# Kernel optimization log

Measured on AMD Instinct MI355X. Metric: run time of the kernel, lower is better.

## Reference

```python
import jax, jax.numpy as jnp
import numpy as np

B = 8192      # batch (num nodes)
D = 256       # embedding dim
K = 8         # positives per node -> nnz = B*K
EPS = 1e-8


def setup_inputs() -> dict:
    key = jax.random.key(0)
    k_emb, k_val = jax.random.split(key)
    embeddings = jax.random.normal(k_emb, (B, D), dtype=jnp.float32)
    # structured sparse positive mask: node i is positive with (i+1..i+K) mod B
    # -> unique pairs, row-major sorted (coalesced), no self loops
    rows = jnp.repeat(jnp.arange(B, dtype=jnp.int64), K)           # [B*K]
    offs = jnp.tile(jnp.arange(1, K + 1, dtype=jnp.int64), B)      # [B*K]
    cols = (rows + offs) % B
    pos_vals = jax.random.uniform(k_val, (B * K,), dtype=jnp.float32)
    temperature = jnp.float32(0.5)  # learnable scalar nn.Parameter
    return {
        "embeddings": embeddings,
        "pos_vals": pos_vals,
        "temperature": temperature,
        "pos_row": rows,
        "pos_col": cols,
    }


def reference(embeddings, pos_vals, temperature, pos_row, pos_col):
    n = embeddings.shape[0]
    # F.normalize(p=2, dim=1) with eps=1e-12
    norm = jnp.linalg.norm(embeddings, axis=1, keepdims=True)
    z = embeddings / jnp.maximum(norm, 1e-12)

    temp = jax.nn.softplus(temperature)
    sim = jnp.matmul(z, z.T) / temp                                 # [B,B]
    sim = sim - jax.lax.stop_gradient(jnp.max(sim, axis=1, keepdims=True))

    pos_dense = jnp.zeros((n, n), dtype=bool).at[pos_row, pos_col].set(True)
    identity = jnp.eye(n, dtype=bool)
    neg_mask = (~pos_dense) & (~identity)

    # pos weights: 'inverse_sim' -> 1 - values, min-max normalized
    pos_w = 1.0 - pos_vals
    pos_w = (pos_w - jnp.min(pos_w)) / (jnp.max(pos_w) - jnp.min(pos_w) + EPS)

    # neg weights: 'inverse_sim' -> min-max over negative sims, +1; weight_mat=1 elsewhere
    neg_min = jnp.min(jnp.where(neg_mask, sim, jnp.inf))
    neg_max = jnp.max(jnp.where(neg_mask, sim, -jnp.inf))
    neg_w = (sim - neg_min) / (neg_max - neg_min + EPS) + 1.0
    log_weight = jnp.where(neg_mask, jnp.log(neg_w), 0.0)

    log_probs = sim - jax.nn.logsumexp(sim + log_weight, axis=1, keepdims=True)

    pos_log = log_probs[pos_row, pos_col]   # same ordering as torch boolean index (coalesced mask)
    loss = -jnp.mean(pos_log * pos_w)
    return loss
```

## Files before the change

kernel.cpp:

```cpp
#include <hip/hip_runtime.h>

#define NB 8192
#define ND 256
#define NMASK 8191
#define CEPS 1e-8f
#define L2E 1.4426950408889634f
#define LN2 0.6931471805599453f
#define SC1 0x7F7F7F7F

#if __has_builtin(__builtin_amdgcn_exp2f)
#define EXP2(x) __builtin_amdgcn_exp2f(x)
#else
#define EXP2(x) exp2f(x)
#endif

typedef float f32x4 __attribute__((ext_vector_type(4)));
typedef int v8i __attribute__((ext_vector_type(8)));
typedef int v4i __attribute__((ext_vector_type(4)));
union V8 { v8i v; v4i q[2]; };


__global__ void k_norm(const float* __restrict__ emb, const float* __restrict__ temperature,
                       const float* __restrict__ pos_vals, char* __restrict__ zb8,
                       float* __restrict__ bpvmin, float* __restrict__ bpvmax,
                       float* __restrict__ out) {
  const int tid = threadIdx.x, lane = tid & 63, w = tid >> 6;
  const int bid = blockIdx.x;
  if (bid == 0 && tid == 0) out[0] = 0.f;
  float sp = log1pf(expf(temperature[0]));
  float alpha = sqrtf(L2E / sp);
  int row = bid * 4 + w;
  const float4 e = *(const float4*)(emb + row * ND + lane * 4);
  float ss = e.x * e.x + e.y * e.y + e.z * e.z + e.w * e.w;
#pragma unroll
  for (int mk = 1; mk < 64; mk <<= 1) ss += __shfl_xor(ss, mk, 64);
  float rn = alpha / fmaxf(sqrtf(ss), 1e-12f);
  int pk = __builtin_amdgcn_cvt_pk_fp8_f32(e.x * rn, e.y * rn, 0, 0);
  pk = __builtin_amdgcn_cvt_pk_fp8_f32(e.z * rn, e.w * rn, pk, 1);
  *(int*)(zb8 + row * 256 + lane * 4) = pk;
  if (w == 0) {
    float v = (lane < 32) ? pos_vals[bid * 32 + lane] : 0.f;
    float mn = (lane < 32) ? v : INFINITY;
    float mx = (lane < 32) ? v : -INFINITY;
#pragma unroll
    for (int mk = 1; mk < 32; mk <<= 1) {
      mn = fminf(mn, __shfl_xor(mn, mk, 64));
      mx = fmaxf(mx, __shfl_xor(mx, mk, 64));
    }
    if (lane == 0) { bpvmin[bid] = mn; bpvmax[bid] = mx; }
  }
}

__global__ __launch_bounds__(256) void k_gemm(
    const char* __restrict__ zb8, float2* __restrict__ EpR, float2* __restrict__ EpC,
    float* __restrict__ sBand, float* __restrict__ bmin, float* __restrict__ bmax) {
  __shared__ __align__(16) char smem[16384];
  const int tid = threadIdx.x, lane = tid & 63, w = tid >> 6;
  const int l15 = lane & 15, lq = lane >> 4;
  const int bid = blockIdx.x;
  int d, rb;
  if (bid < 2048) { d = bid >> 6; rb = bid & 63; }
  else { d = 32; rb = bid - 2048; }
  const int cb = (rb + d) & 63;
  const int roww = rb * 128 + w * 32;
  const int colbase = cb * 128;

  V8 aF[2][2];
#pragma unroll
  for (int mt = 0; mt < 2; ++mt) {
    const char* ar = zb8 + (roww + mt * 16 + l15) * 256 + lq * 32;
#pragma unroll
    for (int kc = 0; kc < 2; ++kc) {
      aF[mt][kc].q[0] = *(const v4i*)(ar + kc * 128);
      aF[mt][kc].q[1] = *(const v4i*)(ar + kc * 128 + 16);
    }
  }

  float E1r[8], Ear[8];
#pragma unroll
  for (int i = 0; i < 8; ++i) { E1r[i] = 0.f; Ear[i] = 0.f; }
  float2 cA[4][2];
#pragma unroll
  for (int s = 0; s < 4; ++s) { cA[s][0] = make_float2(0.f, 0.f); cA[s][1] = make_float2(0.f, 0.f); }
  float vmn = INFINITY, vmx = -INFINITY;

  const char* gsrc[2];
#pragma unroll
  for (int i = 0; i < 2; ++i) {
    int j = w * 2 + i, T = j >> 1, h = j & 1, nt = T & 1, kc = T >> 1;
    gsrc[i] = zb8 + (colbase + nt * 16 + l15) * 256 + kc * 128 + lq * 32 + h * 16;
  }
#pragma unroll
  for (int i = 0; i < 2; ++i)
    __builtin_amdgcn_global_load_lds(
        (const __attribute__((address_space(1))) void*)(gsrc[i]),
        (__attribute__((address_space(3))) void*)(smem + (w * 2 + i) * 1024), 16, 0, 0);

#pragma unroll
  for (int step = 0; step < 4; ++step) {
    __syncthreads();
    if (step < 3) {
      char* ld = smem + ((step + 1) & 1) * 8192;
#pragma unroll
      for (int i = 0; i < 2; ++i)
        __builtin_amdgcn_global_load_lds(
            (const __attribute__((address_space(1))) void*)(gsrc[i] + (step + 1) * 8192),
            (__attribute__((address_space(3))) void*)(ld + (w * 2 + i) * 1024), 16, 0, 0);
    }
    const char* buf = smem + (step & 1) * 8192;
    f32x4 acc[2][2];
#pragma unroll
    for (int mt = 0; mt < 2; ++mt) {
      acc[mt][0] = (f32x4){0.f, 0.f, 0.f, 0.f};
      acc[mt][1] = (f32x4){0.f, 0.f, 0.f, 0.f};
    }
#pragma unroll
    for (int kc = 0; kc < 2; ++kc) {
      V8 b0, b1;
      b0.q[0] = *(const v4i*)(buf + (kc * 2 + 0) * 2048 + lane * 16);
      b0.q[1] = *(const v4i*)(buf + (kc * 2 + 0) * 2048 + 1024 + lane * 16);
      b1.q[0] = *(const v4i*)(buf + (kc * 2 + 1) * 2048 + lane * 16);
      b1.q[1] = *(const v4i*)(buf + (kc * 2 + 1) * 2048 + 1024 + lane * 16);
#pragma unroll
      for (int mt = 0; mt < 2; ++mt) {
        acc[mt][0] = __builtin_amdgcn_mfma_scale_f32_16x16x128_f8f6f4(
            aF[mt][kc].v, b0.v, acc[mt][0], 0, 0, 0, SC1, 0, SC1);
        acc[mt][1] = __builtin_amdgcn_mfma_scale_f32_16x16x128_f8f6f4(
            aF[mt][kc].v, b1.v, acc[mt][1], 0, 0, 0, SC1, 0, SC1);
      }
    }
    const int offbase = (colbase + step * 32 + l15) - (roww + lq * 4);
    if (d >= 2) {
#pragma unroll
      for (int mt = 0; mt < 2; ++mt)
#pragma unroll
        for (int nt = 0; nt < 2; ++nt)
#pragma unroll
          for (int reg = 0; reg < 4; ++reg) {
            float t = acc[mt][nt][reg];
            float e = EXP2(t);
            E1r[mt * 4 + reg] += e;
            Ear[mt * 4 + reg] = fmaf(e, t, Ear[mt * 4 + reg]);
            cA[step][nt].x += e;
            cA[step][nt].y = fmaf(e, t, cA[step][nt].y);
            vmn = fminf(vmn, t);
            vmx = fmaxf(vmx, t);
          }
    } else if (d == 1) {
#pragma unroll
      for (int mt = 0; mt < 2; ++mt)
#pragma unroll
        for (int nt = 0; nt < 2; ++nt)
#pragma unroll
          for (int reg = 0; reg < 4; ++reg) {
            float t = acc[mt][nt][reg];
            float e = EXP2(t);
            E1r[mt * 4 + reg] += e;
            Ear[mt * 4 + reg] = fmaf(e, t, Ear[mt * 4 + reg]);
            cA[step][nt].x += e;
            cA[step][nt].y = fmaf(e, t, cA[step][nt].y);
            vmn = fminf(vmn, t);
            vmx = fmaxf(vmx, t);
            int off = (offbase + (nt - mt) * 16 - reg) & NMASK;
            if (off <= 8)
              sBand[(roww + mt * 16 + lq * 4 + reg) * 12 + off] = t;
          }
    } else {
#pragma unroll
      for (int mt = 0; mt < 2; ++mt)
#pragma unroll
        for (int nt = 0; nt < 2; ++nt)
#pragma unroll
          for (int reg = 0; reg < 4; ++reg) {
            float t = acc[mt][nt][reg];
            float e = EXP2(t);
            E1r[mt * 4 + reg] += e;
            Ear[mt * 4 + reg] = fmaf(e, t, Ear[mt * 4 + reg]);
            int off = (offbase + (nt - mt) * 16 - reg) & NMASK;
            bool isB = off <= 8;
            vmn = fminf(vmn, isB ? vmn : t);
            vmx = fmaxf(vmx, isB ? vmx : t);
            if (isB)
              sBand[(roww + mt * 16 + lq * 4 + reg) * 12 + off] = t;
          }
    }
  }

#pragma unroll
  for (int mk = 1; mk < 16; mk <<= 1)
#pragma unroll
    for (int i = 0; i < 8; ++i) {
      E1r[i] += __shfl_xor(E1r[i], mk, 64);
      Ear[i] += __shfl_xor(Ear[i], mk, 64);
    }
  if (l15 == 0) {
#pragma unroll
    for (int mt = 0; mt < 2; ++mt)
#pragma unroll
      for (int reg = 0; reg < 4; ++reg) {
        int row = roww + mt * 16 + lq * 4 + reg;
        EpR[d * NB + row] = make_float2(E1r[mt * 4 + reg], Ear[mt * 4 + reg]);
      }
  }
#pragma unroll
  for (int mk = 16; mk < 64; mk <<= 1)
#pragma unroll
    for (int s = 0; s < 4; ++s)
#pragma unroll
      for (int nt = 0; nt < 2; ++nt) {
        cA[s][nt].x += __shfl_xor(cA[s][nt].x, mk, 64);
        cA[s][nt].y += __shfl_xor(cA[s][nt].y, mk, 64);
      }
#pragma unroll
  for (int mk = 1; mk < 64; mk <<= 1) {
    vmn = fminf(vmn, __shfl_xor(vmn, mk, 64));
    vmx = fmaxf(vmx, __shfl_xor(vmx, mk, 64));
  }
  __syncthreads();
  float2* colAcc = (float2*)smem;
  float* redmm = (float*)(smem + 4096);
  if (d != 0 && lq == 0) {
#pragma unroll
    for (int s = 0; s < 4; ++s)
#pragma unroll
      for (int nt = 0; nt < 2; ++nt)
        colAcc[w * 128 + s * 32 + nt * 16 + l15] = cA[s][nt];
  }
  if (lane == 0) { redmm[w] = vmn; redmm[4 + w] = vmx; }
  __syncthreads();
  if (d != 0 && tid < 128) {
    float2 a = colAcc[tid], b = colAcc[128 + tid], c = colAcc[256 + tid], e = colAcc[384 + tid];
    EpC[d * NB + colbase + tid] = make_float2(a.x + b.x + c.x + e.x, a.y + b.y + c.y + e.y);
  }
  if (tid == 0) {
    bmin[bid] = fminf(fminf(redmm[0], redmm[1]), fminf(redmm[2], redmm[3]));
    bmax[bid] = fmaxf(fmaxf(redmm[4], redmm[5]), fmaxf(redmm[6], redmm[7]));
  }
}

__global__ void k_final(const float* __restrict__ pos_vals,
                        const float2* __restrict__ EpR, const float2* __restrict__ EpC,
                        const float* __restrict__ sBand,
                        const float* __restrict__ bmin, const float* __restrict__ bmax,
                        const float* __restrict__ bpvmin, const float* __restrict__ bpvmax,
                        float* __restrict__ out) {
  const int tid = threadIdx.x, lane = tid & 63, w = tid >> 6;
  __shared__ float sv[16];
  __shared__ float coef[4];
  float mn = INFINITY, mx = -INFINITY, pmn = INFINITY, pmx = -INFINITY;
  for (int i = tid; i < 2080; i += 256) { mn = fminf(mn, bmin[i]); mx = fmaxf(mx, bmax[i]); }
  for (int i = tid; i < 2048; i += 256) { pmn = fminf(pmn, bpvmin[i]); pmx = fmaxf(pmx, bpvmax[i]); }
#pragma unroll
  for (int mk = 1; mk < 64; mk <<= 1) {
    mn = fminf(mn, __shfl_xor(mn, mk, 64));
    mx = fmaxf(mx, __shfl_xor(mx, mk, 64));
    pmn = fminf(pmn, __shfl_xor(pmn, mk, 64));
    pmx = fmaxf(pmx, __shfl_xor(pmx, mk, 64));
  }
  if (lane == 0) { sv[w] = mn; sv[4 + w] = mx; sv[8 + w] = pmn; sv[12 + w] = pmx; }
  __syncthreads();
  if (tid == 0) {
    float tmin = fminf(fminf(sv[0], sv[1]), fminf(sv[2], sv[3]));
    float tmax = fmaxf(fmaxf(sv[4], sv[5]), fmaxf(sv[6], sv[7]));
    float pvmin = fminf(fminf(sv[8], sv[9]), fminf(sv[10], sv[11]));
    float pvmax = fmaxf(fmaxf(sv[12], sv[13]), fmaxf(sv[14], sv[15]));
    float At = LN2 / ((tmax - tmin) * LN2 + CEPS);
    coef[0] = At;
    coef[1] = 1.f - At * tmin;
    coef[2] = pvmax;
    coef[3] = 1.f / (pvmax - pvmin + CEPS);
  }
  __syncthreads();
  const float At = coef[0], Bt = coef[1], pvmax = coef[2], pwInv = coef[3];

  int row = blockIdx.x * 256 + tid;
  float e1 = 0.f, ea = 0.f;
#pragma unroll
  for (int dd = 0; dd < 32; ++dd) { float2 p = EpR[dd * NB + row]; e1 += p.x; ea += p.y; }
#pragma unroll
  for (int dd = 1; dd < 32; ++dd) { float2 p = EpC[dd * NB + row]; e1 += p.x; ea += p.y; }
  {
    float2 p = (row < 4096) ? EpR[32 * NB + row] : EpC[32 * NB + row];
    e1 += p.x; ea += p.y;
  }
  float tb[9], Sb = 0.f, Sbt = 0.f;
#pragma unroll
  for (int o = 0; o <= 8; ++o) {
    tb[o] = sBand[row * 12 + o];
    float e = EXP2(tb[o]);
    Sb += e;
    Sbt = fmaf(e, tb[o], Sbt);
  }
  float denom = At * (ea - Sbt) + Bt * (e1 - Sb) + Sb;
  float lse = logf(denom);
  float contrib = 0.f;
#pragma unroll
  for (int k = 0; k < 8; ++k) {
    float v = pos_vals[row * 8 + k];
    contrib += (pvmax - v) * pwInv * (tb[k + 1] * LN2 - lse);
  }
#pragma unroll
  for (int mk = 1; mk < 64; mk <<= 1) contrib += __shfl_xor(contrib, mk, 64);
  __syncthreads();
  if (lane == 0) sv[w] = contrib;
  __syncthreads();
  if (tid == 0)
    atomicAdd(out, -(sv[0] + sv[1] + sv[2] + sv[3]) * (1.0f / 65536.0f));
}

extern "C" void kernel_launch(void* const* d_in, const int* in_sizes, int n_in,
                              void* d_out, int out_size, void* d_ws, size_t ws_size,
                              hipStream_t stream) {
  const float* emb = (const float*)d_in[0];
  const float* pos_vals = (const float*)d_in[1];
  const float* temperature = (const float*)d_in[2];
  float* out = (float*)d_out;

  char* ws = (char*)d_ws;
  size_t off = 0;
  float2* EpR = (float2*)(ws + off); off += (size_t)33 * NB * 8;
  float2* EpC = (float2*)(ws + off); off += (size_t)33 * NB * 8;
  float* sBand = (float*)(ws + off); off += (size_t)NB * 12 * 4;
  float* bmin = (float*)(ws + off); off += 2080 * 4 + 128;
  float* bmax = (float*)(ws + off); off += 2080 * 4 + 128;
  float* bpvmin = (float*)(ws + off); off += 2048 * 4;
  float* bpvmax = (float*)(ws + off); off += 2048 * 4;
  char* zb8 = (char*)(ws + off); off += (size_t)NB * 256;

  k_norm<<<2048, 256, 0, stream>>>(emb, temperature, pos_vals, zb8, bpvmin, bpvmax, out);
  k_gemm<<<2080, 256, 0, stream>>>(zb8, EpR, EpC, sBand, bmin, bmax);
  k_final<<<32, 256, 0, stream>>>(pos_vals, EpR, EpC, sBand, bmin, bmax, bpvmin, bpvmax, out);
}
```

Measured before the change: 103.4 us.

## Load full column tile into LDS upfront, drop double-buffered per-step pipeline

Replaces the double-buffered 4-step LDS pipeline for the B (column) tile with a single bulk load of the whole 128x256 fp8 column tile into 32KB of shared memory, issued before the A fragments are loaded, followed by one barrier. This removes the per-step __syncthreads and interleaved async loads. In exchange LDS use per block doubles, which may reduce occupancy, and compute can no longer overlap with the later loads.

```diff
diff --git a/kernel.cpp b/kernel.cpp
--- a/kernel.cpp
+++ b/kernel.cpp
@@ -54,7 +54,7 @@
 __global__ __launch_bounds__(256) void k_gemm(
     const char* __restrict__ zb8, float2* __restrict__ EpR, float2* __restrict__ EpC,
     float* __restrict__ sBand, float* __restrict__ bmin, float* __restrict__ bmax) {
-  __shared__ __align__(16) char smem[16384];
+  __shared__ __align__(16) char smem[32768];
   const int tid = threadIdx.x, lane = tid & 63, w = tid >> 6;
   const int l15 = lane & 15, lq = lane >> 4;
   const int bid = blockIdx.x;
@@ -65,6 +65,15 @@
   const int roww = rb * 128 + w * 32;
   const int colbase = cb * 128;
 
+#pragma unroll
+  for (int i = 0; i < 8; ++i) {
+    int s = w * 8 + i, T = s >> 1, h = s & 1, ct = T >> 1, kc = T & 1;
+    const char* g = zb8 + (colbase + ct * 16 + l15) * 256 + kc * 128 + lq * 32 + h * 16;
+    __builtin_amdgcn_global_load_lds(
+        (const __attribute__((address_space(1))) void*)(g),
+        (__attribute__((address_space(3))) void*)(smem + s * 1024), 16, 0, 0);
+  }
+
   V8 aF[2][2];
 #pragma unroll
   for (int mt = 0; mt < 2; ++mt) {
@@ -84,30 +93,10 @@
   for (int s = 0; s < 4; ++s) { cA[s][0] = make_float2(0.f, 0.f); cA[s][1] = make_float2(0.f, 0.f); }
   float vmn = INFINITY, vmx = -INFINITY;
 
-  const char* gsrc[2];
-#pragma unroll
-  for (int i = 0; i < 2; ++i) {
-    int j = w * 2 + i, T = j >> 1, h = j & 1, nt = T & 1, kc = T >> 1;
-    gsrc[i] = zb8 + (colbase + nt * 16 + l15) * 256 + kc * 128 + lq * 32 + h * 16;
-  }
-#pragma unroll
-  for (int i = 0; i < 2; ++i)
-    __builtin_amdgcn_global_load_lds(
-        (const __attribute__((address_space(1))) void*)(gsrc[i]),
-        (__attribute__((address_space(3))) void*)(smem + (w * 2 + i) * 1024), 16, 0, 0);
+  __syncthreads();
 
 #pragma unroll
   for (int step = 0; step < 4; ++step) {
-    __syncthreads();
-    if (step < 3) {
-      char* ld = smem + ((step + 1) & 1) * 8192;
-#pragma unroll
-      for (int i = 0; i < 2; ++i)
-        __builtin_amdgcn_global_load_lds(
-            (const __attribute__((address_space(1))) void*)(gsrc[i] + (step + 1) * 8192),
-            (__attribute__((address_space(3))) void*)(ld + (w * 2 + i) * 1024), 16, 0, 0);
-    }
-    const char* buf = smem + (step & 1) * 8192;
     f32x4 acc[2][2];
 #pragma unroll
     for (int mt = 0; mt < 2; ++mt) {
@@ -117,10 +106,12 @@
 #pragma unroll
     for (int kc = 0; kc < 2; ++kc) {
       V8 b0, b1;
-      b0.q[0] = *(const v4i*)(buf + (kc * 2 + 0) * 2048 + lane * 16);
-      b0.q[1] = *(const v4i*)(buf + (kc * 2 + 0) * 2048 + 1024 + lane * 16);
-      b1.q[0] = *(const v4i*)(buf + (kc * 2 + 1) * 2048 + lane * 16);
-      b1.q[1] = *(const v4i*)(buf + (kc * 2 + 1) * 2048 + 1024 + lane * 16);
+      const char* t0 = smem + ((step * 2 + 0) * 2 + kc) * 2048;
+      const char* t1 = smem + ((step * 2 + 1) * 2 + kc) * 2048;
+      b0.q[0] = *(const v4i*)(t0 + lane * 16);
+      b0.q[1] = *(const v4i*)(t0 + 1024 + lane * 16);
+      b1.q[0] = *(const v4i*)(t1 + lane * 16);
+      b1.q[1] = *(const v4i*)(t1 + 1024 + lane * 16);
 #pragma unroll
       for (int mt = 0; mt < 2; ++mt) {
         acc[mt][0] = __builtin_amdgcn_mfma_scale_f32_16x16x128_f8f6f4(
```

New measurement: 103.0 us. Within noise of the previous version (-0.4%).
